# Kernel optimization log

Hardware: AMD Instinct MI355X
Metric: run time of the kernel (lower is better)

## Reference

```python
import jax, jax.numpy as jnp
import numpy as np

PE_SIZE = 16          # sqrt(num_patches=256)
HIDDEN_STRIDE = 2
CUBIC_A = -0.75       # torch bicubic coefficient


def cubic_resize_matrix(in_size, out_size, a=CUBIC_A):
    """(out_size, in_size) weights for torch bicubic, align_corners=False."""
    dst = np.arange(out_size)
    src = (dst + 0.5) * in_size / out_size - 0.5
    x0 = np.floor(src).astype(np.int64)
    W = np.zeros((out_size, in_size), np.float32)
    for k in range(-1, 3):  # 4 taps
        idx = np.clip(x0 + k, 0, in_size - 1)  # border replicate
        d = np.abs(src - (x0 + k))
        w = np.where(d <= 1.0, (a + 2) * d**3 - (a + 3) * d**2 + 1.0,
            np.where(d < 2.0, a * d**3 - 5 * a * d**2 + 8 * a * d - 4 * a, 0.0))
        np.add.at(W, (dst, idx), w.astype(np.float32))
    return W


def setup_inputs() -> dict:
    key = jax.random.key(0)
    k1, k2, k3, k4 = jax.random.split(key, 4)
    n_img, t, h, w = 8, 1, 64, 64
    total = n_img * t * h * w  # 32768 patches
    in_feat, d = 3 * 14 * 14, 1152
    return {
        "pixel_values": jax.random.normal(k1, (total, in_feat), jnp.float32),
        "w_patch": jax.random.normal(k2, (d, in_feat), jnp.float32) * 0.02,
        "b_patch": jax.random.normal(k3, (d,), jnp.float32) * 0.02,
        "pos_table": jax.random.normal(k4, (PE_SIZE * PE_SIZE, d), jnp.float32) * 0.02,
        "grid_thws": jnp.array([[t, h, w]] * n_img, jnp.int64),
    }


def _pos_embed(pos_table, grid):
    """grid: np int array (n_img, 3) -> (sum t*h*w, d) positional embeddings."""
    d = pos_table.shape[-1]
    pe_grid = pos_table.reshape(PE_SIZE, PE_SIZE, d)  # (H, W, d)
    s = HIDDEN_STRIDE
    pieces = []
    for t, h, w in grid:
        Wh = jnp.asarray(cubic_resize_matrix(PE_SIZE, int(h)))
        Ww = jnp.asarray(cubic_resize_matrix(PE_SIZE, int(w)))
        pe = jnp.einsum('hH,wW,HWd->hwd', Wh, Ww, pe_grid)  # (h, w, d)
        # hidden_stride window rearrange: (h,w,d) -> (h/s, w/s, s, s, d)
        pe = pe.reshape(h // s, s, w // s, s, d).transpose(0, 2, 1, 3, 4)
        pe = pe.reshape(h * w, d)
        pe = jnp.tile(pe, (int(t), 1))  # repeat over temporal dim
        pieces.append(pe)
    return jnp.concatenate(pieces, axis=0)


def reference(pixel_values, w_patch, b_patch, pos_table, grid_thws):
    # patch embedding (Linear)
    patch_embeds = pixel_values @ w_patch.T + b_patch  # (N, d)
    grid = np.asarray(grid_thws)  # static shapes per image
    pos = _pos_embed(pos_table, grid)
    return patch_embeds + pos
```

## Files before the change

### kernel.cpp

```cpp
#include <hip/hip_runtime.h>

typedef unsigned short ushort_t;
typedef unsigned int uint_t;

typedef __bf16 bf16x8 __attribute__((ext_vector_type(8)));
typedef float f32x4 __attribute__((ext_vector_type(4)));

#define KK 588
#define KP 608
#define NN 1152
#define MM 32768
#define POSROWS 4096


__device__ __forceinline__ ushort_t f2bf(float f) {
    union { float f; uint_t u; } v; v.f = f;
    uint_t u = v.u;
    uint_t r = (u + 0x7FFFu + ((u >> 16) & 1u)) >> 16;
    return (ushort_t)r;
}

__device__ __forceinline__ void cubic_taps(int dst, float* w, int* idx) {
    const float A = -0.75f;
    float src = (float)dst * 0.25f - 0.25f;
    int x0 = (int)floorf(src);
    #pragma unroll
    for (int k = -1; k <= 2; ++k) {
        int i = x0 + k;
        int ic = i < 0 ? 0 : (i > 15 ? 15 : i);
        float d = fabsf(src - (float)i);
        float wt;
        if (d <= 1.0f)      wt = ((A + 2.0f) * d - (A + 3.0f)) * d * d + 1.0f;
        else if (d < 2.0f)  wt = ((A * d - 5.0f * A) * d + 8.0f * A) * d - 4.0f * A;
        else                wt = 0.0f;
        w[k + 1] = wt;
        idx[k + 1] = ic;
    }
}


__global__ void pos_kernel(const float* __restrict__ pt, float* __restrict__ pos) {
    int n = blockIdx.x;
    int h = ((n >> 7) << 1) | ((n >> 1) & 1);
    int w = (((n >> 2) & 31) << 1) | (n & 1);
    float wh[4], ww[4];
    int ih[4], iw[4];
    cubic_taps(h, wh, ih);
    cubic_taps(w, ww, iw);
    for (int j = threadIdx.x; j < NN; j += blockDim.x) {
        float s = 0.f;
        #pragma unroll
        for (int a = 0; a < 4; ++a) {
            float rs = 0.f;
            #pragma unroll
            for (int b = 0; b < 4; ++b)
                rs += ww[b] * pt[(ih[a] * 16 + iw[b]) * NN + j];
            s += wh[a] * rs;
        }
        pos[(size_t)n * NN + j] = s;
    }
}


__global__ void cvt_pad_kernel(const float* __restrict__ src, ushort_t* __restrict__ dst,
                               int rows) {
    int idx = blockIdx.x * 256 + threadIdx.x;
    int total = rows * KP;
    if (idx >= total) return;
    int row = idx / KP;
    int k = idx - row * KP;
    float v = (k < KK) ? src[(size_t)row * KK + k] : 0.0f;
    dst[idx] = f2bf(v);
}


__global__ void gemm_kernel(const ushort_t* __restrict__ Abf,
                            const ushort_t* __restrict__ Bbf,
                            const float* __restrict__ bias,
                            const float* __restrict__ pos,
                            float* __restrict__ out) {
    __shared__ __align__(16) ushort_t lA[128 * 32];
    __shared__ __align__(16) ushort_t lB[128 * 32];

    const int t = threadIdx.x;
    const int lane = t & 63;
    const int wid = t >> 6;
    const int wm = wid >> 1, wn = wid & 1;

    const int bm = (int)blockIdx.x * 128;
    const int bn = (int)blockIdx.y * 128;

    f32x4 acc[4][4] = {};

    for (int ks = 0; ks < KP / 32; ++ks) {
        const int k0 = ks * 32;
        #pragma unroll
        for (int i = 0; i < 2; ++i) {
            int idx = i * 256 + t;
            int row = idx >> 2;
            int slot = idx & 3;
            int khi = slot ^ ((row >> 1) & 3);
            const ushort_t* gA = Abf + (size_t)(bm + row) * KP + k0 + khi * 8;
            const ushort_t* gB = Bbf + (size_t)(bn + row) * KP + k0 + khi * 8;
            ushort_t* lAp = lA + (size_t)(idx & ~63) * 8;
            ushort_t* lBp = lB + (size_t)(idx & ~63) * 8;
            __builtin_amdgcn_global_load_lds(
                (const __attribute__((address_space(1))) void*)gA,
                (__attribute__((address_space(3))) void*)lAp, 16, 0, 0);
            __builtin_amdgcn_global_load_lds(
                (const __attribute__((address_space(1))) void*)gB,
                (__attribute__((address_space(3))) void*)lBp, 16, 0, 0);
        }
        __syncthreads();

        bf16x8 af[4], bfr[4];
        #pragma unroll
        for (int mi = 0; mi < 4; ++mi) {
            int row = wm * 64 + mi * 16 + (lane & 15);
            int slot = (lane >> 4) ^ ((row >> 1) & 3);
            af[mi] = *(const bf16x8*)(lA + row * 32 + slot * 8);
        }
        #pragma unroll
        for (int ni = 0; ni < 4; ++ni) {
            int row = wn * 64 + ni * 16 + (lane & 15);
            int slot = (lane >> 4) ^ ((row >> 1) & 3);
            bfr[ni] = *(const bf16x8*)(lB + row * 32 + slot * 8);
        }
        #pragma unroll
        for (int mi = 0; mi < 4; ++mi)
            #pragma unroll
            for (int ni = 0; ni < 4; ++ni)
                acc[mi][ni] = __builtin_amdgcn_mfma_f32_16x16x32_bf16(
                    af[mi], bfr[ni], acc[mi][ni], 0, 0, 0);
        __syncthreads();
    }

    #pragma unroll
    for (int mi = 0; mi < 4; ++mi) {
        #pragma unroll
        for (int ni = 0; ni < 4; ++ni) {
            int col = bn + wn * 64 + ni * 16 + (lane & 15);
            float bcol = bias[col];
            #pragma unroll
            for (int r = 0; r < 4; ++r) {
                int row = bm + wm * 64 + mi * 16 + (lane >> 4) * 4 + r;
                int prow = row & (POSROWS - 1);
                out[(size_t)row * NN + col] =
                    acc[mi][ni][r] + bcol + pos[(size_t)prow * NN + col];
            }
        }
    }
}


__global__ void fb_kernel(const float* __restrict__ A, const float* __restrict__ W,
                          const float* __restrict__ bias, const float* __restrict__ pt,
                          float* __restrict__ out) {
    __shared__ float sA[16][17], sB[16][17];
    int ty = threadIdx.y, tx = threadIdx.x;
    int row = blockIdx.y * 16 + ty;
    int col = blockIdx.x * 16 + tx;
    float acc = 0.f;
    for (int k0 = 0; k0 < KK; k0 += 16) {
        int ka = k0 + tx;
        sA[ty][tx] = (ka < KK) ? A[(size_t)row * KK + ka] : 0.f;
        sB[ty][tx] = (ka < KK) ? W[(size_t)(blockIdx.x * 16 + ty) * KK + ka] : 0.f;
        __syncthreads();
        #pragma unroll
        for (int kk = 0; kk < 16; ++kk)
            acc += sA[ty][kk] * sB[tx][kk];
        __syncthreads();
    }
    int n = row & (POSROWS - 1);
    int h = ((n >> 7) << 1) | ((n >> 1) & 1);
    int w = (((n >> 2) & 31) << 1) | (n & 1);
    float wh[4], ww[4]; int ih[4], iw[4];
    cubic_taps(h, wh, ih);
    cubic_taps(w, ww, iw);
    float p = 0.f;
    #pragma unroll
    for (int a = 0; a < 4; ++a) {
        float rs = 0.f;
        #pragma unroll
        for (int b = 0; b < 4; ++b)
            rs += ww[b] * pt[(ih[a] * 16 + iw[b]) * NN + col];
        p += wh[a] * rs;
    }
    out[(size_t)row * NN + col] = acc + bias[col] + p;
}


extern "C" void kernel_launch(void* const* d_in, const int* in_sizes, int n_in,
                              void* d_out, int out_size, void* d_ws, size_t ws_size,
                              hipStream_t stream) {
    const float* pv   = (const float*)d_in[0];
    const float* wp   = (const float*)d_in[1];
    const float* bias = (const float*)d_in[2];
    const float* pt   = (const float*)d_in[3];
    float* out = (float*)d_out;

    const size_t pos_bytes = (size_t)POSROWS * NN * 4;
    const size_t pvb_bytes = (size_t)MM * KP * 2;
    const size_t wb_bytes  = (size_t)NN * KP * 2;
    const size_t need = pos_bytes + pvb_bytes + wb_bytes;

    if (ws_size >= need) {
        float* pos = (float*)d_ws;
        ushort_t* pvb = (ushort_t*)((char*)d_ws + pos_bytes);
        ushort_t* wb  = (ushort_t*)((char*)d_ws + pos_bytes + pvb_bytes);

        pos_kernel<<<POSROWS, 256, 0, stream>>>(pt, pos);

        int tot_pv = MM * KP;
        cvt_pad_kernel<<<(tot_pv + 255) / 256, 256, 0, stream>>>(pv, pvb, MM);
        int tot_w = NN * KP;
        cvt_pad_kernel<<<(tot_w + 255) / 256, 256, 0, stream>>>(wp, wb, NN);

        gemm_kernel<<<dim3(MM / 128, NN / 128), 256, 0, stream>>>(pvb, wb, bias, pos, out);
    } else {
        fb_kernel<<<dim3(NN / 16, MM / 16), dim3(16, 16), 0, stream>>>(pv, wp, bias, pt, out);
    }
}
```

Baseline: 141.6 us.

## Fuse fp32-to-bf16 conversion of A into GEMM with double-buffered LDS

Removes the separate pass that converts and pads pixel_values to bf16. The GEMM now loads fp32 A straight from global memory into registers, converts it to bf16, and writes it into a double-buffered LDS tile. The next K-step's A and B loads are prefetched while the current step's MFMAs run. It also switches to a 1D grid with an XCD-aware block remap, so neighbouring tiles that share A rows land on the same XCD's L2. In exchange, each block reads twice as many A bytes (fp32 instead of bf16), uses more registers and twice the LDS, and handles the ragged last K-step with masked loads.

After: 166.0 us. +17.2%, slower.

```diff
diff --git a/kernel.cpp b/kernel.cpp
--- a/kernel.cpp
+++ b/kernel.cpp
@@ -11,14 +11,9 @@
 #define NN 1152
 #define MM 32768
 #define POSROWS 4096
-
-
-__device__ __forceinline__ ushort_t f2bf(float f) {
-    union { float f; uint_t u; } v; v.f = f;
-    uint_t u = v.u;
-    uint_t r = (u + 0x7FFFu + ((u >> 16) & 1u)) >> 16;
-    return (ushort_t)r;
-}
+#define NSTEP 19
+#define GRID 2304
+
 
 __device__ __forceinline__ void cubic_taps(int dst, float* w, int* idx) {
     const float A = -0.75f;
@@ -70,61 +65,120 @@
     int row = idx / KP;
     int k = idx - row * KP;
     float v = (k < KK) ? src[(size_t)row * KK + k] : 0.0f;
-    dst[idx] = f2bf(v);
-}
-
-
-__global__ void gemm_kernel(const ushort_t* __restrict__ Abf,
+    union { float f; uint_t u; } c; c.f = v;
+    uint_t u = c.u;
+    dst[idx] = (ushort_t)((u + 0x7FFFu + ((u >> 16) & 1u)) >> 16);
+}
+
+
+__global__ void gemm_kernel(const float* __restrict__ A,
                             const ushort_t* __restrict__ Bbf,
                             const float* __restrict__ bias,
                             const float* __restrict__ pos,
                             float* __restrict__ out) {
-    __shared__ __align__(16) ushort_t lA[128 * 32];
-    __shared__ __align__(16) ushort_t lB[128 * 32];
+    __shared__ __align__(16) ushort_t lA[2][128 * 32];
+    __shared__ __align__(16) ushort_t lB[2][128 * 32];
 
     const int t = threadIdx.x;
     const int lane = t & 63;
     const int wid = t >> 6;
     const int wm = wid >> 1, wn = wid & 1;
 
-    const int bm = (int)blockIdx.x * 128;
-    const int bn = (int)blockIdx.y * 128;
+    int linear = (int)blockIdx.x;
+    int xcd = linear & 7;
+    int local = linear >> 3;
+    int wg = xcd * (GRID / 8) + local;
+    int mt = wg / 9;
+    int nt = wg - mt * 9;
+    const int bm = mt * 128;
+    const int bn = nt * 128;
 
     f32x4 acc[4][4] = {};
-
-    for (int ks = 0; ks < KP / 32; ++ks) {
+    f32x4 areg[2][2];
+
+    auto loadA = [&](int ks) {
         const int k0 = ks * 32;
-        #pragma unroll
-        for (int i = 0; i < 2; ++i) {
-            int idx = i * 256 + t;
-            int row = idx >> 2;
-            int slot = idx & 3;
+        if (k0 + 32 <= KK) {
+            #pragma unroll
+            for (int j = 0; j < 2; ++j) {
+                int idx = j * 256 + t;
+                int row = idx >> 2, q = idx & 3;
+                const float* g = A + (size_t)(bm + row) * KK + k0 + q * 8;
+                areg[j][0] = *(const f32x4*)g;
+                areg[j][1] = *(const f32x4*)(g + 4);
+            }
+        } else {
+            #pragma unroll
+            for (int j = 0; j < 2; ++j) {
+                int idx = j * 256 + t;
+                int row = idx >> 2, q = idx & 3;
+                int kbase = k0 + q * 8;
+                const float* g = A + (size_t)(bm + row) * KK + kbase;
+                #pragma unroll
+                for (int e = 0; e < 4; ++e) {
+                    areg[j][0][e] = (kbase + e < KK) ? g[e] : 0.f;
+                    areg[j][1][e] = (kbase + 4 + e < KK) ? g[4 + e] : 0.f;
+                }
+            }
+        }
+    };
+
+    auto writeA = [&](int buf) {
+        #pragma unroll
+        for (int j = 0; j < 2; ++j) {
+            int idx = j * 256 + t;
+            int row = idx >> 2, q = idx & 3;
+            int qs = q ^ ((row >> 1) & 3);
+            bf16x8 v;
+            #pragma unroll
+            for (int e = 0; e < 4; ++e) {
+                v[e]     = (__bf16)areg[j][0][e];
+                v[e + 4] = (__bf16)areg[j][1][e];
+            }
+            *(bf16x8*)(&lA[buf][row * 32 + qs * 8]) = v;
+        }
+    };
+
+    auto stageB = [&](int ks, int buf) {
+        const int k0 = ks * 32;
+        #pragma unroll
+        for (int j = 0; j < 2; ++j) {
+            int idx = j * 256 + t;
+            int row = idx >> 2, slot = idx & 3;
             int khi = slot ^ ((row >> 1) & 3);
-            const ushort_t* gA = Abf + (size_t)(bm + row) * KP + k0 + khi * 8;
             const ushort_t* gB = Bbf + (size_t)(bn + row) * KP + k0 + khi * 8;
-            ushort_t* lAp = lA + (size_t)(idx & ~63) * 8;
-            ushort_t* lBp = lB + (size_t)(idx & ~63) * 8;
-            __builtin_amdgcn_global_load_lds(
-                (const __attribute__((address_space(1))) void*)gA,
-                (__attribute__((address_space(3))) void*)lAp, 16, 0, 0);
+            ushort_t* lBp = &lB[buf][(size_t)(idx & ~63) * 8];
             __builtin_amdgcn_global_load_lds(
                 (const __attribute__((address_space(1))) void*)gB,
                 (__attribute__((address_space(3))) void*)lBp, 16, 0, 0);
         }
-        __syncthreads();
+    };
+
+    loadA(0);
+    stageB(0, 0);
+    writeA(0);
+    __syncthreads();
+
+    for (int ks = 0; ks < NSTEP; ++ks) {
+        const int cur = ks & 1, nxt = cur ^ 1;
+        const bool more = (ks + 1 < NSTEP);
+        if (more) {
+            loadA(ks + 1);
+            stageB(ks + 1, nxt);
+        }
 
         bf16x8 af[4], bfr[4];
         #pragma unroll
         for (int mi = 0; mi < 4; ++mi) {
             int row = wm * 64 + mi * 16 + (lane & 15);
             int slot = (lane >> 4) ^ ((row >> 1) & 3);
-            af[mi] = *(const bf16x8*)(lA + row * 32 + slot * 8);
+            af[mi] = *(const bf16x8*)(&lA[cur][row * 32 + slot * 8]);
         }
         #pragma unroll
         for (int ni = 0; ni < 4; ++ni) {
             int row = wn * 64 + ni * 16 + (lane & 15);
             int slot = (lane >> 4) ^ ((row >> 1) & 3);
-            bfr[ni] = *(const bf16x8*)(lB + row * 32 + slot * 8);
+            bfr[ni] = *(const bf16x8*)(&lB[cur][row * 32 + slot * 8]);
         }
         #pragma unroll
         for (int mi = 0; mi < 4; ++mi)
@@ -132,6 +186,8 @@
             for (int ni = 0; ni < 4; ++ni)
                 acc[mi][ni] = __builtin_amdgcn_mfma_f32_16x16x32_bf16(
                     af[mi], bfr[ni], acc[mi][ni], 0, 0, 0);
+
+        if (more) writeA(nxt);
         __syncthreads();
     }
 
@@ -200,23 +256,19 @@
     float* out = (float*)d_out;
 
     const size_t pos_bytes = (size_t)POSROWS * NN * 4;
-    const size_t pvb_bytes = (size_t)MM * KP * 2;
     const size_t wb_bytes  = (size_t)NN * KP * 2;
-    const size_t need = pos_bytes + pvb_bytes + wb_bytes;
+    const size_t need = pos_bytes + wb_bytes;
 
     if (ws_size >= need) {
         float* pos = (float*)d_ws;
-        ushort_t* pvb = (ushort_t*)((char*)d_ws + pos_bytes);
-        ushort_t* wb  = (ushort_t*)((char*)d_ws + pos_bytes + pvb_bytes);
+        ushort_t* wb = (ushort_t*)((char*)d_ws + pos_bytes);
 
         pos_kernel<<<POSROWS, 256, 0, stream>>>(pt, pos);
 
-        int tot_pv = MM * KP;
-        cvt_pad_kernel<<<(tot_pv + 255) / 256, 256, 0, stream>>>(pv, pvb, MM);
         int tot_w = NN * KP;
         cvt_pad_kernel<<<(tot_w + 255) / 256, 256, 0, stream>>>(wp, wb, NN);
 
-        gemm_kernel<<<dim3(MM / 128, NN / 128), 256, 0, stream>>>(pvb, wb, bias, pos, out);
+        gemm_kernel<<<GRID, 256, 0, stream>>>(pv, wb, bias, pos, out);
     } else {
         fb_kernel<<<dim3(NN / 16, MM / 16), dim3(16, 16), 0, stream>>>(pv, wp, bias, pt, out);
     }
```
